# Optimization experiments

Measured on AMD Instinct MI355X. Metric: run time of the kernel, lower is better.

## Reference

```python
import jax, jax.numpy as jnp
import numpy as np

B = 32
HID = 2048
INNER = 4096       # expand_factor * hidden_size
NHEADS = 8
HEAD = INNER // NHEADS   # 512
KCONV = 4
CAP = 30.0         # gate_soft_cap
EPS = 1e-6
GN_EPS = 1e-5      # torch GroupNorm default eps


def setup_inputs() -> dict:
    key = jax.random.key(0)
    ks = jax.random.split(key, 12)
    s = 0.02
    return {
        "x": jax.random.normal(ks[0], (B, HID), jnp.float32),
        "conv_state": jax.random.normal(ks[1], (B, INNER, KCONV - 1), jnp.float32),
        "cell_state": jax.random.normal(ks[2], (B, NHEADS, HEAD, HEAD), jnp.float32) * 0.1,
        "norm_state": jax.random.normal(ks[3], (B, NHEADS, HEAD), jnp.float32) * 0.1,
        "max_state": jnp.zeros((B, NHEADS), jnp.float32),
        "rms_w": jnp.ones((HID,), jnp.float32),
        "Wx": jax.random.normal(ks[4], (INNER, HID), jnp.float32) * s,
        "Wg": jax.random.normal(ks[5], (INNER, HID), jnp.float32) * s,
        "Wqkv": jax.random.normal(ks[6], (3 * INNER, INNER), jnp.float32) * s,
        "conv_w": jax.random.normal(ks[7], (INNER, KCONV), jnp.float32) * s,
        "conv_b": jnp.zeros((INNER,), jnp.float32),
        "Wi": jax.random.normal(ks[8], (NHEADS, 3 * INNER), jnp.float32) * s,
        "bi": jnp.full((NHEADS,), -10.0, jnp.float32),
        "Wf": jax.random.normal(ks[9], (NHEADS, 3 * INNER), jnp.float32) * s,
        "bf": jnp.zeros((NHEADS,), jnp.float32),
        "gn_w": jnp.ones((INNER,), jnp.float32),
        "gn_b": jnp.zeros((INNER,), jnp.float32),
        "Wdown": jax.random.normal(ks[10], (HID, INNER), jnp.float32) * s,
        "skip_w": jnp.ones((INNER,), jnp.float32),
    }


def reference(x, conv_state, cell_state, norm_state, max_state,
              rms_w, Wx, Wg, Wqkv, conv_w, conv_b, Wi, bi, Wf, bf,
              gn_w, gn_b, Wdown, skip_w):
    skip = x
    # RMSNorm
    xn = x * jax.lax.rsqrt(jnp.mean(x * x, -1, keepdims=True) + EPS) * rms_w
    x_mlstm = xn @ Wx.T          # [B, INNER]
    x_gate = xn @ Wg.T           # [B, INNER]
    # depthwise causal conv over (state | current step)
    x_cat = jnp.concatenate([conv_state, x_mlstm[:, :, None]], -1)  # [B, INNER, K]
    x_conv = jnp.einsum('bck,ck->bc', x_cat, conv_w) + conv_b
    new_conv_state = x_cat[:, :, 1:]
    xmc = jax.nn.silu(x_conv)
    qkv = xmc @ Wqkv.T           # [B, 3*INNER] == cat(q,k,v)
    q, k, v = jnp.split(qkv, 3, axis=1)
    # gates (soft-capped)
    ig = CAP * jnp.tanh((qkv @ Wi.T + bi) / CAP)   # [B, H]
    fg = CAP * jnp.tanh((qkv @ Wf.T + bf) / CAP)
    qh = q.reshape(B, NHEADS, HEAD)
    kh = k.reshape(B, NHEADS, HEAD) / np.float32(np.sqrt(HEAD))
    vh = v.reshape(B, NHEADS, HEAD)
    log_f = jax.nn.log_sigmoid(fg)
    max_new = jnp.maximum(ig, max_state + log_f)
    i_gate = jnp.exp(ig - max_new)
    f_gate = jnp.exp(log_f + max_state - max_new)
    # outer-product state update
    cell_new = (f_gate[:, :, None, None] * cell_state
                + i_gate[:, :, None, None] * (kh[..., :, None] * vh[..., None, :]))
    norm_new = f_gate[..., None] * norm_state + i_gate[..., None] * kh
    # per-head readout
    numer = jnp.einsum('bhd,bhde->bhe', qh, cell_new)
    qn = jnp.sum(qh * norm_new, -1)                 # [B, H]
    denom = jnp.maximum(jnp.abs(qn), jnp.exp(-max_new)) + EPS
    out = numer / denom[..., None]                  # [B, H, d]
    # GroupNorm with num_groups = NHEADS over flattened channels
    mu = jnp.mean(out, -1, keepdims=True)
    var = jnp.mean((out - mu) ** 2, -1, keepdims=True)
    out = (out - mu) * jax.lax.rsqrt(var + GN_EPS)
    out = out.reshape(B, INNER) * gn_w + gn_b
    h = (out + skip_w * xmc) * jax.nn.silu(x_gate)
    y = h @ Wdown.T + skip
    return y, new_conv_state, cell_new, norm_new, max_new
```

## Files before the change

### kernel.cpp

```cpp
#include <hip/hip_runtime.h>
#include <hip/hip_bf16.h>

#define B_      32
#define HID_    2048
#define INNER_  4096
#define NH_     8
#define HEAD_   512
#define CAP_    30.0f
#define DCH_    64

typedef short short8 __attribute__((ext_vector_type(8)));
typedef float f32x4 __attribute__((ext_vector_type(4)));

static __device__ __forceinline__ unsigned short f2bf(float f) {
    unsigned int u = __float_as_uint(f);
    u = (u + 0x7fffu + ((u >> 16) & 1u)) >> 16;
    return (unsigned short)u;
}

static __device__ __forceinline__ float sigm(float x) { return 1.0f / (1.0f + expf(-x)); }
static __device__ __forceinline__ float silu(float x) { return x * sigm(x); }

__global__ void k_rms(const float* __restrict__ x, const float* __restrict__ rms_w,
                      float* __restrict__ xn) {
    const int b = blockIdx.x, t = threadIdx.x;
    __shared__ float red[4];
    const float* xr = x + b * HID_;
    float s = 0.f;
    for (int i = t; i < HID_; i += 256) { float v = xr[i]; s += v * v; }
    for (int off = 32; off; off >>= 1) s += __shfl_down(s, off, 64);
    if ((t & 63) == 0) red[t >> 6] = s;
    __syncthreads();
    const float scale = rsqrtf((red[0] + red[1] + red[2] + red[3]) / (float)HID_ + 1e-6f);
    float* xo = xn + b * HID_;
    for (int i = t; i < HID_; i += 256) xo[i] = xr[i] * scale * rms_w[i];
}

__global__ __launch_bounds__(256) void k_gemm(const float* __restrict__ A,
                       const float* __restrict__ W,
                       float* __restrict__ C, int N, int K, int Kper) {
    __shared__ unsigned short Al[32][136];
    __shared__ unsigned short Wl[64][136];
    const int tid  = threadIdx.x;
    const int lane = tid & 63;
    const int wave = tid >> 6;
    const int quad = lane >> 4;
    const int l16  = lane & 15;
    const int oBlk = blockIdx.x * 64;
    const int k0s  = blockIdx.y * Kper;
    const int ntiles = Kper >> 7;

    f32x4 acc0 = {0.f, 0.f, 0.f, 0.f};
    f32x4 acc1 = {0.f, 0.f, 0.f, 0.f};

    for (int kt = 0; kt < ntiles; ++kt) {
        const int k0 = k0s + kt * 128;
        for (int i = tid; i < 1024; i += 256) {
            const int r = i >> 5, c = i & 31;
            const float4 f = *(const float4*)(A + r * K + k0 + c * 4);
            ushort4 u; u.x = f2bf(f.x); u.y = f2bf(f.y); u.z = f2bf(f.z); u.w = f2bf(f.w);
            *(ushort4*)&Al[r][c * 4] = u;
        }
        for (int i = tid; i < 2048; i += 256) {
            const int r = i >> 5, c = i & 31;
            const float4 f = *(const float4*)(W + (size_t)(oBlk + r) * K + k0 + c * 4);
            ushort4 u; u.x = f2bf(f.x); u.y = f2bf(f.y); u.z = f2bf(f.z); u.w = f2bf(f.w);
            *(ushort4*)&Wl[r][c * 4] = u;
        }
        __syncthreads();
        #pragma unroll
        for (int ks = 0; ks < 4; ++ks) {
            const int kk = ks * 32 + quad * 8;
            const short8 a0 = *(const short8*)&Al[l16][kk];
            const short8 a1 = *(const short8*)&Al[16 + l16][kk];
            const short8 wf = *(const short8*)&Wl[wave * 16 + l16][kk];
            acc0 = __builtin_amdgcn_mfma_f32_16x16x32_bf16(a0, wf, acc0, 0, 0, 0);
            acc1 = __builtin_amdgcn_mfma_f32_16x16x32_bf16(a1, wf, acc1, 0, 0, 0);
        }
        __syncthreads();
    }
    const int o = oBlk + wave * 16 + l16;
    #pragma unroll
    for (int r = 0; r < 4; ++r) {
        const int b0 = quad * 4 + r;
        atomicAdd(&C[(size_t)b0 * N + o], acc0[r]);
        atomicAdd(&C[(size_t)(16 + b0) * N + o], acc1[r]);
    }
}

__global__ void k_conv(const float* __restrict__ xm, const float* __restrict__ conv_state,
                       const float* __restrict__ conv_w, const float* __restrict__ conv_b,
                       float* __restrict__ xmc, float* __restrict__ ncs_out) {
    const int idx = blockIdx.x * 256 + threadIdx.x;
    if (idx >= B_ * INNER_) return;
    const int c = idx & (INNER_ - 1);
    const float* cs = conv_state + (size_t)idx * 3;
    const float c0 = cs[0], c1 = cs[1], c2 = cs[2];
    const float xv = xm[idx];
    const float* w = conv_w + c * 4;
    const float conv = c0 * w[0] + c1 * w[1] + c2 * w[2] + xv * w[3] + conv_b[c];
    xmc[idx] = silu(conv);
    float* no = ncs_out + (size_t)idx * 3;
    no[0] = c1; no[1] = c2; no[2] = xv;
}

__global__ void k_gates(const float* __restrict__ qkv, const float* __restrict__ Wi,
                        const float* __restrict__ bi, const float* __restrict__ Wf,
                        const float* __restrict__ bfv, const float* __restrict__ max_state,
                        const float* __restrict__ norm_state,
                        float* __restrict__ ig_ws, float* __restrict__ fg_ws,
                        float* __restrict__ max_new, float* __restrict__ norm_out,
                        float* __restrict__ denom_ws) {
    const int bh = blockIdx.x, b = bh >> 3, h = bh & 7, t = threadIdx.x;
    const float* q  = qkv + (size_t)b * (3 * INNER_);
    const float* wi = Wi + (size_t)h * (3 * INNER_);
    const float* wf = Wf + (size_t)h * (3 * INNER_);
    float si = 0.f, sf = 0.f;
    for (int j = t; j < 3 * INNER_; j += 256) {
        const float v = q[j];
        si += v * wi[j];
        sf += v * wf[j];
    }
    __shared__ float r1[4], r2[4], sc[3];
    for (int off = 32; off; off >>= 1) {
        si += __shfl_down(si, off, 64);
        sf += __shfl_down(sf, off, 64);
    }
    if ((t & 63) == 0) { r1[t >> 6] = si; r2[t >> 6] = sf; }
    __syncthreads();
    if (t == 0) {
        float ig = r1[0] + r1[1] + r1[2] + r1[3] + bi[h];
        float fg = r2[0] + r2[1] + r2[2] + r2[3] + bfv[h];
        ig = CAP_ * tanhf(ig / CAP_);
        fg = CAP_ * tanhf(fg / CAP_);
        const float logf_ = (fg >= 0.f) ? -log1pf(expf(-fg)) : (fg - log1pf(expf(fg)));
        const float ms = max_state[bh];
        const float mn = fmaxf(ig, ms + logf_);
        const float i_g = expf(ig - mn);
        const float f_g = expf(logf_ + ms - mn);
        max_new[bh] = mn; ig_ws[bh] = i_g; fg_ws[bh] = f_g;
        sc[0] = i_g; sc[1] = f_g; sc[2] = mn;
    }
    __syncthreads();
    const float i_g = sc[0], f_g = sc[1], mx = sc[2];
    const float rs = 0.044194173824159216f;
    const float* qr = q + h * HEAD_;
    const float* kr = qr + INNER_;
    const float* ns = norm_state + (size_t)bh * HEAD_;
    float qn = 0.f;
    for (int d = t; d < HEAD_; d += 256) {
        const float qv = qr[d];
        const float nn = f_g * ns[d] + i_g * (kr[d] * rs);
        norm_out[(size_t)bh * HEAD_ + d] = nn;
        qn += qv * nn;
    }
    for (int off = 32; off; off >>= 1) qn += __shfl_down(qn, off, 64);
    if ((t & 63) == 0) r1[t >> 6] = qn;
    __syncthreads();
    if (t == 0) {
        const float q_total = r1[0] + r1[1] + r1[2] + r1[3];
        denom_ws[bh] = fmaxf(fabsf(q_total), expf(-mx)) + 1e-6f;
    }
}

__global__ __launch_bounds__(256) void k_cell(const float* __restrict__ qkv,
                       const float* __restrict__ ig_ws, const float* __restrict__ fg_ws,
                       const float* __restrict__ cell_state,
                       float* __restrict__ cell_out, float* __restrict__ numer_ws) {
    const int blk = blockIdx.x;
    const int bh = blk >> 3, chunk = blk & 7;
    const int b = bh >> 3, h = bh & 7, t = threadIdx.x;
    const int d0 = chunk * DCH_;
    __shared__ float q_l[DCH_], ik_l[DCH_];
    __shared__ float nred[HEAD_];
    const float i_g = ig_ws[bh], f_g = fg_ws[bh];
    const float rs = 0.044194173824159216f;
    const float* qr = qkv + (size_t)b * (3 * INNER_) + h * HEAD_;
    const float* kr = qr + INNER_;
    const float* vr = qr + 2 * INNER_;
    if (t < DCH_) {
        q_l[t]  = qr[d0 + t];
        ik_l[t] = i_g * (kr[d0 + t] * rs);
    }
    __syncthreads();
    const int half = t >> 7;
    const int col  = (t & 127) * 4;
    const float4 v4 = *(const float4*)(vr + col);
    const float* pin  = cell_state + (size_t)bh * HEAD_ * HEAD_ + (size_t)(d0 + half) * HEAD_ + col;
    float*       pout = cell_out   + (size_t)bh * HEAD_ * HEAD_ + (size_t)(d0 + half) * HEAD_ + col;
    float4 num = {0.f, 0.f, 0.f, 0.f};
    #pragma unroll 4
    for (int it = 0; it < DCH_ / 2; ++it) {
        const int d = it * 2 + half;
        const float4 c4 = *(const float4*)pin;
        const float ik = ik_l[d], qv = q_l[d];
        float4 cn;
        cn.x = f_g * c4.x + ik * v4.x;
        cn.y = f_g * c4.y + ik * v4.y;
        cn.z = f_g * c4.z + ik * v4.z;
        cn.w = f_g * c4.w + ik * v4.w;
        *(float4*)pout = cn;
        num.x += qv * cn.x; num.y += qv * cn.y; num.z += qv * cn.z; num.w += qv * cn.w;
        pin  += 2 * HEAD_;
        pout += 2 * HEAD_;
    }
    if (half == 0) {
        nred[col] = num.x; nred[col+1] = num.y; nred[col+2] = num.z; nred[col+3] = num.w;
    }
    __syncthreads();
    if (half == 1) {
        float* nw = numer_ws + (size_t)bh * HEAD_;
        atomicAdd(&nw[col],     nred[col]     + num.x);
        atomicAdd(&nw[col + 1], nred[col + 1] + num.y);
        atomicAdd(&nw[col + 2], nred[col + 2] + num.z);
        atomicAdd(&nw[col + 3], nred[col + 3] + num.w);
    }
}

__global__ void k_epi(const float* __restrict__ numer_ws, const float* __restrict__ denom_ws,
                      const float* __restrict__ gn_w, const float* __restrict__ gn_b,
                      const float* __restrict__ skip_w, const float* __restrict__ xmc,
                      const float* __restrict__ x_gate, float* __restrict__ h_out) {
    const int bh = blockIdx.x, b = bh >> 3, h = bh & 7, t = threadIdx.x;
    __shared__ float redA[4], redB[4];
    const float denom = denom_ws[bh];
    const float* nu = numer_ws + (size_t)bh * HEAD_;
    float s = 0.f, s2 = 0.f;
    for (int e = t; e < HEAD_; e += 256) {
        const float o = nu[e] / denom;
        s += o; s2 += o * o;
    }
    for (int off = 32; off; off >>= 1) {
        s  += __shfl_down(s, off, 64);
        s2 += __shfl_down(s2, off, 64);
    }
    if ((t & 63) == 0) { redA[t >> 6] = s; redB[t >> 6] = s2; }
    __syncthreads();
    const float mu  = (redA[0] + redA[1] + redA[2] + redA[3]) / (float)HEAD_;
    const float ex2 = (redB[0] + redB[1] + redB[2] + redB[3]) / (float)HEAD_;
    const float inv = rsqrtf(fmaxf(ex2 - mu * mu, 0.f) + 1e-5f);
    for (int e = t; e < HEAD_; e += 256) {
        const int i = h * HEAD_ + e;
        const float og = (nu[e] / denom - mu) * inv * gn_w[i] + gn_b[i];
        const float xg = x_gate[(size_t)b * INNER_ + i];
        const float hv = (og + skip_w[i] * xmc[(size_t)b * INNER_ + i]) * silu(xg);
        h_out[(size_t)b * INNER_ + i] = hv;
    }
}

extern "C" void kernel_launch(void* const* d_in, const int* in_sizes, int n_in,
                              void* d_out, int out_size, void* d_ws, size_t ws_size,
                              hipStream_t stream) {
    const float* x          = (const float*)d_in[0];
    const float* conv_state = (const float*)d_in[1];
    const float* cell_state = (const float*)d_in[2];
    const float* norm_state = (const float*)d_in[3];
    const float* max_state  = (const float*)d_in[4];
    const float* rms_w      = (const float*)d_in[5];
    const float* Wx         = (const float*)d_in[6];
    const float* Wg         = (const float*)d_in[7];
    const float* Wqkv       = (const float*)d_in[8];
    const float* conv_w     = (const float*)d_in[9];
    const float* conv_b     = (const float*)d_in[10];
    const float* Wi         = (const float*)d_in[11];
    const float* bi         = (const float*)d_in[12];
    const float* Wf         = (const float*)d_in[13];
    const float* bfv        = (const float*)d_in[14];
    const float* gn_w       = (const float*)d_in[15];
    const float* gn_b       = (const float*)d_in[16];
    const float* Wdown      = (const float*)d_in[17];
    const float* skip_w     = (const float*)d_in[18];

    float* out = (float*)d_out;
    float* y_out    = out;
    float* ncs_out  = y_out + B_ * HID_;
    float* cell_out = ncs_out + (size_t)B_ * INNER_ * 3;
    float* norm_out = cell_out + (size_t)B_ * NH_ * HEAD_ * HEAD_;
    float* max_out  = norm_out + (size_t)B_ * NH_ * HEAD_;

    float* w = (float*)d_ws;
    float* xn       = w;
    float* xmc      = xn + B_ * HID_;
    float* h_ws     = xmc + B_ * INNER_;
    float* ig_ws    = h_ws + B_ * INNER_;
    float* fg_ws    = ig_ws + B_ * NH_;
    float* denom_ws = fg_ws + B_ * NH_;
    float* x_mlstm  = denom_ws + B_ * NH_;
    float* x_gate   = x_mlstm + B_ * INNER_;
    float* qkv      = x_gate + B_ * INNER_;
    float* numer_ws = qkv + B_ * 3 * INNER_;

    hipMemsetAsync(x_mlstm, 0,
                   (size_t)(2 * B_ * INNER_ + B_ * 3 * INNER_ + B_ * NH_ * HEAD_) * 4, stream);
    hipMemcpyAsync(y_out, x, (size_t)B_ * HID_ * 4, hipMemcpyDeviceToDevice, stream);

    k_rms<<<B_, 256, 0, stream>>>(x, rms_w, xn);

    k_gemm<<<dim3(INNER_ / 64, 8), 256, 0, stream>>>(xn, Wx, x_mlstm, INNER_, HID_, HID_ / 8);
    k_gemm<<<dim3(INNER_ / 64, 8), 256, 0, stream>>>(xn, Wg, x_gate, INNER_, HID_, HID_ / 8);

    k_conv<<<(B_ * INNER_) / 256, 256, 0, stream>>>(x_mlstm, conv_state, conv_w, conv_b,
                                                    xmc, ncs_out);

    k_gemm<<<dim3(3 * INNER_ / 64, 8), 256, 0, stream>>>(xmc, Wqkv, qkv,
                                                         3 * INNER_, INNER_, INNER_ / 8);

    k_gates<<<B_ * NH_, 256, 0, stream>>>(qkv, Wi, bi, Wf, bfv, max_state, norm_state,
                                          ig_ws, fg_ws, max_out, norm_out, denom_ws);

    k_cell<<<B_ * NH_ * 8, 256, 0, stream>>>(qkv, ig_ws, fg_ws, cell_state,
                                             cell_out, numer_ws);

    k_epi<<<B_ * NH_, 256, 0, stream>>>(numer_ws, denom_ws, gn_w, gn_b, skip_w,
                                        xmc, x_gate, h_ws);

    k_gemm<<<dim3(HID_ / 64, 16), 256, 0, stream>>>(h_ws, Wdown, y_out, HID_, INNER_, INNER_ / 16);
}
```

Measured before the change: 719.5 us.

## Replace atomic split-K accumulation with partial buffers and fused reduction kernels

Split-K GEMMs now write their partial results to per-slice buffers instead of atomically adding into zeroed outputs. Small reduction kernels sum the partials, with the x_mlstm/x_gate sums folded into the conv kernel and the residual add folded into the final reduction. This removes the memset and device copy. The Wx and Wg GEMMs are merged into one launch through grid z. Weight and cell-state streams use nontemporal loads and stores, and the k_cell numerator partials are reduced inside k_epi. The cost is extra partial-buffer traffic and two more kernel launches.

```diff
diff --git a/kernel.cpp b/kernel.cpp
--- a/kernel.cpp
+++ b/kernel.cpp
@@ -37,8 +37,11 @@
 }
 
 __global__ __launch_bounds__(256) void k_gemm(const float* __restrict__ A,
-                       const float* __restrict__ W,
-                       float* __restrict__ C, int N, int K, int Kper) {
+                       const float* __restrict__ W0, float* __restrict__ C0,
+                       const float* __restrict__ W1, float* __restrict__ C1,
+                       int N, int K, int Kper) {
+    const float* __restrict__ W = blockIdx.z ? W1 : W0;
+    float* __restrict__ C = blockIdx.z ? C1 : C0;
     __shared__ unsigned short Al[32][136];
     __shared__ unsigned short Wl[64][136];
     const int tid  = threadIdx.x;
@@ -63,8 +66,9 @@
         }
         for (int i = tid; i < 2048; i += 256) {
             const int r = i >> 5, c = i & 31;
-            const float4 f = *(const float4*)(W + (size_t)(oBlk + r) * K + k0 + c * 4);
-            ushort4 u; u.x = f2bf(f.x); u.y = f2bf(f.y); u.z = f2bf(f.z); u.w = f2bf(f.w);
+            const f32x4 f = __builtin_nontemporal_load(
+                (const f32x4*)(W + (size_t)(oBlk + r) * K + k0 + c * 4));
+            ushort4 u; u.x = f2bf(f[0]); u.y = f2bf(f[1]); u.z = f2bf(f[2]); u.w = f2bf(f[3]);
             *(ushort4*)&Wl[r][c * 4] = u;
         }
         __syncthreads();
@@ -80,28 +84,49 @@
         __syncthreads();
     }
     const int o = oBlk + wave * 16 + l16;
+    float* Cr = C + (size_t)(blockIdx.y * 32) * N + o;
     #pragma unroll
     for (int r = 0; r < 4; ++r) {
         const int b0 = quad * 4 + r;
-        atomicAdd(&C[(size_t)b0 * N + o], acc0[r]);
-        atomicAdd(&C[(size_t)(16 + b0) * N + o], acc1[r]);
-    }
-}
-
-__global__ void k_conv(const float* __restrict__ xm, const float* __restrict__ conv_state,
+        Cr[(size_t)b0 * N]        = acc0[r];
+        Cr[(size_t)(16 + b0) * N] = acc1[r];
+    }
+}
+
+__global__ __launch_bounds__(256) void k_convred(const float* __restrict__ xm_p,
+                       const float* __restrict__ xg_p,
+                       const float* __restrict__ conv_state,
                        const float* __restrict__ conv_w, const float* __restrict__ conv_b,
-                       float* __restrict__ xmc, float* __restrict__ ncs_out) {
+                       float* __restrict__ xmc, float* __restrict__ ncs_out,
+                       float* __restrict__ x_gate) {
     const int idx = blockIdx.x * 256 + threadIdx.x;
-    if (idx >= B_ * INNER_) return;
     const int c = idx & (INNER_ - 1);
+    float xm = 0.f, xg = 0.f;
+    #pragma unroll
+    for (int s = 0; s < 8; ++s) {
+        xm += xm_p[(size_t)s * (B_ * INNER_) + idx];
+        xg += xg_p[(size_t)s * (B_ * INNER_) + idx];
+    }
+    x_gate[idx] = xg;
     const float* cs = conv_state + (size_t)idx * 3;
     const float c0 = cs[0], c1 = cs[1], c2 = cs[2];
-    const float xv = xm[idx];
     const float* w = conv_w + c * 4;
-    const float conv = c0 * w[0] + c1 * w[1] + c2 * w[2] + xv * w[3] + conv_b[c];
+    const float conv = c0 * w[0] + c1 * w[1] + c2 * w[2] + xm * w[3] + conv_b[c];
     xmc[idx] = silu(conv);
     float* no = ncs_out + (size_t)idx * 3;
-    no[0] = c1; no[1] = c2; no[2] = xv;
+    no[0] = c1; no[1] = c2; no[2] = xm;
+}
+
+__global__ __launch_bounds__(256) void k_qkvred(const float* __restrict__ qkv_p,
+                                                float* __restrict__ qkv) {
+    const int e = (blockIdx.x * 256 + threadIdx.x) * 4;
+    float4 s = {0.f, 0.f, 0.f, 0.f};
+    #pragma unroll
+    for (int p = 0; p < 8; ++p) {
+        const float4 v = *(const float4*)(qkv_p + (size_t)p * (B_ * 3 * INNER_) + e);
+        s.x += v.x; s.y += v.y; s.z += v.z; s.w += v.w;
+    }
+    *(float4*)(qkv + e) = s;
 }
 
 __global__ void k_gates(const float* __restrict__ qkv, const float* __restrict__ Wi,
@@ -166,7 +191,7 @@
 __global__ __launch_bounds__(256) void k_cell(const float* __restrict__ qkv,
                        const float* __restrict__ ig_ws, const float* __restrict__ fg_ws,
                        const float* __restrict__ cell_state,
-                       float* __restrict__ cell_out, float* __restrict__ numer_ws) {
+                       float* __restrict__ cell_out, float* __restrict__ numer_p) {
     const int blk = blockIdx.x;
     const int bh = blk >> 3, chunk = blk & 7;
     const int b = bh >> 3, h = bh & 7, t = threadIdx.x;
@@ -189,45 +214,51 @@
     const float* pin  = cell_state + (size_t)bh * HEAD_ * HEAD_ + (size_t)(d0 + half) * HEAD_ + col;
     float*       pout = cell_out   + (size_t)bh * HEAD_ * HEAD_ + (size_t)(d0 + half) * HEAD_ + col;
     float4 num = {0.f, 0.f, 0.f, 0.f};
-    #pragma unroll 4
+    #pragma unroll 8
     for (int it = 0; it < DCH_ / 2; ++it) {
         const int d = it * 2 + half;
-        const float4 c4 = *(const float4*)pin;
+        const f32x4 c4 = __builtin_nontemporal_load((const f32x4*)pin);
         const float ik = ik_l[d], qv = q_l[d];
-        float4 cn;
-        cn.x = f_g * c4.x + ik * v4.x;
-        cn.y = f_g * c4.y + ik * v4.y;
-        cn.z = f_g * c4.z + ik * v4.z;
-        cn.w = f_g * c4.w + ik * v4.w;
-        *(float4*)pout = cn;
-        num.x += qv * cn.x; num.y += qv * cn.y; num.z += qv * cn.z; num.w += qv * cn.w;
+        f32x4 cn;
+        cn[0] = f_g * c4[0] + ik * v4.x;
+        cn[1] = f_g * c4[1] + ik * v4.y;
+        cn[2] = f_g * c4[2] + ik * v4.z;
+        cn[3] = f_g * c4[3] + ik * v4.w;
+        __builtin_nontemporal_store(cn, (f32x4*)pout);
+        num.x += qv * cn[0]; num.y += qv * cn[1]; num.z += qv * cn[2]; num.w += qv * cn[3];
         pin  += 2 * HEAD_;
         pout += 2 * HEAD_;
     }
     if (half == 0) {
-        nred[col] = num.x; nred[col+1] = num.y; nred[col+2] = num.z; nred[col+3] = num.w;
+        *(float4*)&nred[col] = *(float4*)&num;
     }
     __syncthreads();
     if (half == 1) {
-        float* nw = numer_ws + (size_t)bh * HEAD_;
-        atomicAdd(&nw[col],     nred[col]     + num.x);
-        atomicAdd(&nw[col + 1], nred[col + 1] + num.y);
-        atomicAdd(&nw[col + 2], nred[col + 2] + num.z);
-        atomicAdd(&nw[col + 3], nred[col + 3] + num.w);
-    }
-}
-
-__global__ void k_epi(const float* __restrict__ numer_ws, const float* __restrict__ denom_ws,
+        float4 tot;
+        tot.x = nred[col]     + num.x;
+        tot.y = nred[col + 1] + num.y;
+        tot.z = nred[col + 2] + num.z;
+        tot.w = nred[col + 3] + num.w;
+        *(float4*)(numer_p + ((size_t)bh * 8 + chunk) * HEAD_ + col) = tot;
+    }
+}
+
+__global__ void k_epi(const float* __restrict__ numer_p, const float* __restrict__ denom_ws,
                       const float* __restrict__ gn_w, const float* __restrict__ gn_b,
                       const float* __restrict__ skip_w, const float* __restrict__ xmc,
                       const float* __restrict__ x_gate, float* __restrict__ h_out) {
     const int bh = blockIdx.x, b = bh >> 3, h = bh & 7, t = threadIdx.x;
     __shared__ float redA[4], redB[4];
-    const float denom = denom_ws[bh];
-    const float* nu = numer_ws + (size_t)bh * HEAD_;
+    __shared__ float nu_s[HEAD_];
+    const float inv_d = 1.0f / denom_ws[bh];
+    const float* np = numer_p + (size_t)bh * 8 * HEAD_;
     float s = 0.f, s2 = 0.f;
     for (int e = t; e < HEAD_; e += 256) {
-        const float o = nu[e] / denom;
+        float nu = 0.f;
+        #pragma unroll
+        for (int c = 0; c < 8; ++c) nu += np[c * HEAD_ + e];
+        const float o = nu * inv_d;
+        nu_s[e] = o;
         s += o; s2 += o * o;
     }
     for (int off = 32; off; off >>= 1) {
@@ -241,11 +272,24 @@
     const float inv = rsqrtf(fmaxf(ex2 - mu * mu, 0.f) + 1e-5f);
     for (int e = t; e < HEAD_; e += 256) {
         const int i = h * HEAD_ + e;
-        const float og = (nu[e] / denom - mu) * inv * gn_w[i] + gn_b[i];
+        const float og = (nu_s[e] - mu) * inv * gn_w[i] + gn_b[i];
         const float xg = x_gate[(size_t)b * INNER_ + i];
         const float hv = (og + skip_w[i] * xmc[(size_t)b * INNER_ + i]) * silu(xg);
         h_out[(size_t)b * INNER_ + i] = hv;
     }
+}
+
+__global__ __launch_bounds__(256) void k_yred(const float* __restrict__ y_p,
+                                              const float* __restrict__ x,
+                                              float* __restrict__ y) {
+    const int e = (blockIdx.x * 256 + threadIdx.x) * 4;
+    float4 s = *(const float4*)(x + e);
+    #pragma unroll
+    for (int p = 0; p < 16; ++p) {
+        const float4 v = *(const float4*)(y_p + (size_t)p * (B_ * HID_) + e);
+        s.x += v.x; s.y += v.y; s.z += v.z; s.w += v.w;
+    }
+    *(float4*)(y + e) = s;
 }
 
 extern "C" void kernel_launch(void* const* d_in, const int* in_sizes, int n_in,
@@ -282,37 +326,41 @@
     float* xn       = w;
     float* xmc      = xn + B_ * HID_;
     float* h_ws     = xmc + B_ * INNER_;
-    float* ig_ws    = h_ws + B_ * INNER_;
+    float* x_gate   = h_ws + B_ * INNER_;
+    float* ig_ws    = x_gate + B_ * INNER_;
     float* fg_ws    = ig_ws + B_ * NH_;
     float* denom_ws = fg_ws + B_ * NH_;
-    float* x_mlstm  = denom_ws + B_ * NH_;
-    float* x_gate   = x_mlstm + B_ * INNER_;
-    float* qkv      = x_gate + B_ * INNER_;
-    float* numer_ws = qkv + B_ * 3 * INNER_;
-
-    hipMemsetAsync(x_mlstm, 0,
-                   (size_t)(2 * B_ * INNER_ + B_ * 3 * INNER_ + B_ * NH_ * HEAD_) * 4, stream);
-    hipMemcpyAsync(y_out, x, (size_t)B_ * HID_ * 4, hipMemcpyDeviceToDevice, stream);
+    float* qkv      = denom_ws + B_ * NH_;
+    float* xm_p     = qkv + B_ * 3 * INNER_;
+    float* xg_p     = xm_p + 8 * B_ * INNER_;
+    float* qkv_p    = xg_p + 8 * B_ * INNER_;
+    float* y_p      = qkv_p + (size_t)8 * B_ * 3 * INNER_;
+    float* numer_p  = y_p + 16 * B_ * HID_;
 
     k_rms<<<B_, 256, 0, stream>>>(x, rms_w, xn);
 
-    k_gemm<<<dim3(INNER_ / 64, 8), 256, 0, stream>>>(xn, Wx, x_mlstm, INNER_, HID_, HID_ / 8);
-    k_gemm<<<dim3(INNER_ / 64, 8), 256, 0, stream>>>(xn, Wg, x_gate, INNER_, HID_, HID_ / 8);
-
-    k_conv<<<(B_ * INNER_) / 256, 256, 0, stream>>>(x_mlstm, conv_state, conv_w, conv_b,
-                                                    xmc, ncs_out);
-
-    k_gemm<<<dim3(3 * INNER_ / 64, 8), 256, 0, stream>>>(xmc, Wqkv, qkv,
-                                                         3 * INNER_, INNER_, INNER_ / 8);
+    k_gemm<<<dim3(INNER_ / 64, 8, 2), 256, 0, stream>>>(xn, Wx, xm_p, Wg, xg_p,
+                                                        INNER_, HID_, HID_ / 8);
+
+    k_convred<<<(B_ * INNER_) / 256, 256, 0, stream>>>(xm_p, xg_p, conv_state,
+                                                       conv_w, conv_b, xmc, ncs_out, x_gate);
+
+    k_gemm<<<dim3(3 * INNER_ / 64, 8, 1), 256, 0, stream>>>(xmc, Wqkv, qkv_p, Wqkv, qkv_p,
+                                                            3 * INNER_, INNER_, INNER_ / 8);
+
+    k_qkvred<<<(B_ * 3 * INNER_) / 1024, 256, 0, stream>>>(qkv_p, qkv);
 
     k_gates<<<B_ * NH_, 256, 0, stream>>>(qkv, Wi, bi, Wf, bfv, max_state, norm_state,
                                           ig_ws, fg_ws, max_out, norm_out, denom_ws);
 
     k_cell<<<B_ * NH_ * 8, 256, 0, stream>>>(qkv, ig_ws, fg_ws, cell_state,
-                                             cell_out, numer_ws);
-
-    k_epi<<<B_ * NH_, 256, 0, stream>>>(numer_ws, denom_ws, gn_w, gn_b, skip_w,
+                                             cell_out, numer_p);
+
+    k_epi<<<B_ * NH_, 256, 0, stream>>>(numer_p, denom_ws, gn_w, gn_b, skip_w,
                                         xmc, x_gate, h_ws);
 
-    k_gemm<<<dim3(HID_ / 64, 16), 256, 0, stream>>>(h_ws, Wdown, y_out, HID_, INNER_, INNER_ / 16);
-}
+    k_gemm<<<dim3(HID_ / 64, 16, 1), 256, 0, stream>>>(h_ws, Wdown, y_p, Wdown, y_p,
+                                                       HID_, INNER_, INNER_ / 16);
+
+    k_yred<<<(B_ * HID_) / 1024, 256, 0, stream>>>(y_p, x, y_out);
+}
```

Result: faster. 688.6 us (-4.3%).
